# Performance work log

Measured on AMD Instinct MI355X. Metric: run time of the kernel, lower is better.

## Reference

```python
import jax, jax.numpy as jnp
import numpy as np

DIM = 1024
HEADS = 16
DIM_HEAD = 64
INNER = HEADS * DIM_HEAD
SCALE = DIM_HEAD ** -0.5


def rotate_half(t):
    # '... (j d) -> ... j d' with j=2: split last dim in half
    x1, x2 = jnp.split(t, 2, axis=-1)
    return jnp.concatenate((-x2, x1), axis=-1)


def rotary_pos(n, d, dtype):
    inv_freq = 1.0 / (10000.0 ** (jnp.arange(0, d, 2, dtype=jnp.float32) / d))
    freqs = jnp.arange(n, dtype=jnp.float32)[:, None] * inv_freq[None, :]  # (n, d/2)
    return jnp.concatenate((freqs, freqs), axis=-1).astype(dtype)  # (n, d)


def apply_rope(pos, t):
    return t * jnp.cos(pos) + rotate_half(t) * jnp.sin(pos)


def setup_inputs() -> dict:
    key = jax.random.key(0)
    ks = jax.random.split(key, 5)
    x = jax.random.normal(ks[0], (2, 2048, DIM), dtype=jnp.float32)
    gamma = jnp.ones((DIM,), dtype=jnp.float32)
    beta = jnp.zeros((DIM,), dtype=jnp.float32)
    Wq = jax.random.normal(ks[1], (DIM, INNER), dtype=jnp.float32) * 0.02
    Wkv = jax.random.normal(ks[2], (DIM, 2 * INNER), dtype=jnp.float32) * 0.02
    Wo = jax.random.normal(ks[3], (INNER, DIM), dtype=jnp.float32) * 0.02
    return {"x": x, "gamma": gamma, "beta": beta, "Wq": Wq, "Wkv": Wkv, "Wo": Wo}


def reference(x, gamma, beta, Wq, Wkv, Wo):
    b, n, _ = x.shape
    # LayerNorm with learned gamma, fixed-zero beta buffer
    mu = jnp.mean(x, axis=-1, keepdims=True)
    var = jnp.var(x, axis=-1, keepdims=True)
    xn = (x - mu) / jnp.sqrt(var + 1e-5) * gamma + beta

    q = xn @ Wq                       # (b, n, inner)
    kv = xn @ Wkv
    k, v = jnp.split(kv, 2, axis=-1)

    def to_heads(t):
        return t.reshape(b, n, HEADS, DIM_HEAD).transpose(0, 2, 1, 3)  # b h n d

    q, k, v = map(to_heads, (q, k, v))

    pos = rotary_pos(n, DIM_HEAD, x.dtype)  # (n, d)
    q = apply_rope(pos, q)
    k = apply_rope(pos, k)

    q = q * SCALE
    sim = jnp.einsum('bhid,bhjd->bhij', q, k)

    neg = -jnp.finfo(sim.dtype).max
    causal_mask = jnp.triu(jnp.ones((n, n), dtype=bool), k=1)
    sim = jnp.where(causal_mask, neg, sim)

    attn = jax.nn.softmax(sim, axis=-1)
    out = jnp.einsum('bhij,bhjd->bhid', attn, v)
    out = out.transpose(0, 2, 1, 3).reshape(b, n, INNER)
    return out @ Wo
```

## Files before the change

### kernel.cpp

```cpp
#include <hip/hip_runtime.h>
#include <stdint.h>

typedef unsigned short u16;
typedef __attribute__((ext_vector_type(8))) short short8;
typedef __attribute__((ext_vector_type(4))) float floatx4;
typedef __attribute__((ext_vector_type(4))) unsigned short u16x4;
typedef __attribute__((ext_vector_type(2))) unsigned int uint2v;

__device__ __forceinline__ float bf2f(u16 v) {
  union { uint32_t u; float f; } x; x.u = ((uint32_t)v) << 16; return x.f;
}
__device__ __forceinline__ u16 f2bf(float f) {
  union { float f; uint32_t u; } x; x.f = f;
  uint32_t r = x.u + 0x7fffu + ((x.u >> 16) & 1u);
  return (u16)(r >> 16);
}
__device__ __forceinline__ uint32_t fu(float f) {
  union { float f; uint32_t u; } x; x.f = f; return x.u;
}

#define GL2LDS(g, l)                                                          \
  __builtin_amdgcn_global_load_lds(                                           \
      (const __attribute__((address_space(1))) void*)(g),                     \
      (__attribute__((address_space(3))) void*)(l), 16, 0, 0)

__global__ __launch_bounds__(256) void prep_k(const float* __restrict__ x,
                                              const float* __restrict__ gamma,
                                              const float* __restrict__ beta,
                                              const float* __restrict__ Wq,
                                              const float* __restrict__ Wkv,
                                              const float* __restrict__ Wo,
                                              u16* __restrict__ xn,
                                              u16* __restrict__ wqkvT,
                                              u16* __restrict__ woT) {
  int bid = blockIdx.x;
  int t = threadIdx.x;
  if (bid < 4096) {
    int row = bid;
    const float* xr = x + (size_t)row * 1024;
    float4 xv = *(const float4*)(xr + t * 4);
    float v0 = xv.x, v1 = xv.y, v2 = xv.z, v3 = xv.w;
    float s = v0 + v1 + v2 + v3;
    float s2 = v0 * v0 + v1 * v1 + v2 * v2 + v3 * v3;
#pragma unroll
    for (int d = 1; d < 64; d <<= 1) {
      s += __shfl_xor(s, d, 64);
      s2 += __shfl_xor(s2, d, 64);
    }
    __shared__ float red[8];
    int lane = t & 63, wv = t >> 6;
    if (lane == 0) { red[wv] = s; red[4 + wv] = s2; }
    __syncthreads();
    s = red[0] + red[1] + red[2] + red[3];
    s2 = red[4] + red[5] + red[6] + red[7];
    float mu = s * (1.0f / 1024.0f);
    float var = s2 * (1.0f / 1024.0f) - mu * mu;
    float rstd = rsqrtf(var + 1e-5f);
    float4 gv = *(const float4*)(gamma + t * 4);
    float4 bv = *(const float4*)(beta + t * 4);
    u16x4 ov;
    ov.x = f2bf((v0 - mu) * rstd * gv.x + bv.x);
    ov.y = f2bf((v1 - mu) * rstd * gv.y + bv.y);
    ov.z = f2bf((v2 - mu) * rstd * gv.z + bv.z);
    ov.w = f2bf((v3 - mu) * rstd * gv.w + bv.w);
    *(u16x4*)(xn + (size_t)row * 1024 + t * 4) = ov;
  } else {
    __shared__ float tile[32][33];
    int wb = bid - 4096;
    const float* in;
    u16* outp;
    int C;
    if (wb < 1024) { in = Wq; outp = wqkvT; C = 1024; }
    else if (wb < 3072) { wb -= 1024; in = Wkv; outp = wqkvT + 1024 * 1024; C = 2048; }
    else { wb -= 3072; in = Wo; outp = woT; C = 1024; }
    int nbx = C >> 5;
    int c0 = (wb % nbx) * 32, r0 = (wb / nbx) * 32;
    int tx = t & 31, ty = t >> 5;
#pragma unroll
    for (int i = 0; i < 32; i += 8)
      tile[ty + i][tx] = in[(size_t)(r0 + ty + i) * C + c0 + tx];
    __syncthreads();
#pragma unroll
    for (int i = 0; i < 32; i += 8)
      outp[(size_t)(c0 + ty + i) * 1024 + r0 + tx] = f2bf(tile[tx][ty + i]);
  }
}

__global__ __launch_bounds__(256) void gemm_qkv_k(const u16* __restrict__ A,
                                                  const u16* __restrict__ BT,
                                                  u16* __restrict__ C) {
  const int K = 1024, lda = 1024, ldc = 3072;
  __shared__ __align__(16) u16 lA[2][128 * 32];
  __shared__ __align__(16) u16 lB[2][128 * 32];
  int tid = threadIdx.x;
  int bm = blockIdx.y * 128;
  int bn = blockIdx.x * 128;
  int w = tid >> 6, l = tid & 63;
  int wm = (w >> 1) * 64, wn = (w & 1) * 64;
  int lr = l & 15, lq = l >> 4;
  floatx4 acc[4][4] = {};
  int sr = w * 16 + (l >> 2);
  int sc = (l & 3) * 8;
  int sds = sr * 32 + sc;
  const u16* pA0 = A + (size_t)(bm + sr) * lda + sc;
  const u16* pA1 = pA0 + (size_t)64 * lda;
  const u16* pB0 = BT + (size_t)(bn + sr) * K + sc;
  const u16* pB1 = pB0 + (size_t)64 * K;
  int ao[4], bo[4];
#pragma unroll
  for (int i = 0; i < 4; i++) {
    ao[i] = (wm + i * 16 + lr) * 32 + lq * 8;
    bo[i] = (wn + i * 16 + lr) * 32 + lq * 8;
  }

#define STAGE_QKV(bi)                                                         \
  {                                                                           \
    GL2LDS(pA0, &lA[bi][sds]);                                                \
    GL2LDS(pA1, &lA[bi][sds + 2048]);                                         \
    GL2LDS(pB0, &lB[bi][sds]);                                                \
    GL2LDS(pB1, &lB[bi][sds + 2048]);                                         \
    pA0 += 32; pA1 += 32; pB0 += 32; pB1 += 32;                               \
  }
#define COMPUTE_QKV(bi)                                                       \
  {                                                                           \
    short8 afr[4], bfr[4];                                                    \
    _Pragma("unroll") for (int i = 0; i < 4; i++)                             \
        afr[i] = *(const short8*)(&lA[bi][ao[i]]);                            \
    _Pragma("unroll") for (int i = 0; i < 4; i++)                             \
        bfr[i] = *(const short8*)(&lB[bi][bo[i]]);                            \
    _Pragma("unroll") for (int mi = 0; mi < 4; mi++)                          \
        _Pragma("unroll") for (int ni = 0; ni < 4; ni++)                      \
            acc[mi][ni] = __builtin_amdgcn_mfma_f32_16x16x32_bf16(            \
                afr[mi], bfr[ni], acc[mi][ni], 0, 0, 0);                      \
  }

  STAGE_QKV(0);
  __syncthreads();
#pragma unroll 1
  for (int t = 0; t < 16; ++t) {
    STAGE_QKV(1);
    COMPUTE_QKV(0);
    __syncthreads();
    if (t < 15) STAGE_QKV(0);
    COMPUTE_QKV(1);
    __syncthreads();
  }

  int sec = bn >> 10;
  if (sec == 2) {
#pragma unroll
    for (int mi = 0; mi < 4; mi++)
#pragma unroll
      for (int ni = 0; ni < 4; ni++) {
        int col = bn + wn + ni * 16 + lr;
        int cv = col - 2048;
        int row = bm + wm + mi * 16 + lq * 4;
        int bq = row >> 11;
        int n = row & 2047;
        int bh = (bq << 4) | (cv >> 6);
        int d = cv & 63;
        size_t L = ((size_t)(bh * 64 + d) << 11) + n;
        u16x4 ov;
        ov.x = f2bf(acc[mi][ni][0]);
        ov.y = f2bf(acc[mi][ni][1]);
        ov.z = f2bf(acc[mi][ni][2]);
        ov.w = f2bf(acc[mi][ni][3]);
        *(u16x4*)(C + (L >> 10) * 3072 + 2048 + (L & 1023)) = ov;
      }
  } else {
    float QS = (sec == 0) ? 0.125f * 1.44269504088896f : 1.0f;
#pragma unroll
    for (int ni = 0; ni < 2; ni++) {
      int i = ni * 16 + lr;
      float invf = exp2f(-(float)i * 0.4152410118609203f);
#pragma unroll
      for (int mi = 0; mi < 4; mi++)
#pragma unroll
        for (int r = 0; r < 4; r++) {
          int row = bm + wm + mi * 16 + lq * 4 + r;
          int n = row & 2047;
          float ang = (float)n * invf;
          float s_, c_;
          __sincosf(ang, &s_, &c_);
          float x1 = acc[mi][ni][r], x2 = acc[mi][ni + 2][r];
          int col = bn + wn + ni * 16 + lr;
          C[(size_t)row * ldc + col] = f2bf((x1 * c_ - x2 * s_) * QS);
          C[(size_t)row * ldc + col + 32] = f2bf((x2 * c_ + x1 * s_) * QS);
        }
    }
  }
}

__global__ __launch_bounds__(256) void gemm64_bf16_k(const u16* __restrict__ A,
                                                     const u16* __restrict__ BT,
                                                     float* __restrict__ C,
                                                     int K, int lda, int ldc) {
  __shared__ __align__(16) u16 lA[2][64 * 32];
  __shared__ __align__(16) u16 lB[2][128 * 32];
  int tid = threadIdx.x;
  int bm = blockIdx.y * 64;
  int bn = blockIdx.x * 128;
  int w = tid >> 6, l = tid & 63;
  int wm = (w >> 1) * 32, wn = (w & 1) * 64;
  int lr = l & 15, lq = l >> 4;
  floatx4 acc[2][4] = {};
  int sr = w * 16 + (l >> 2);
  int sc = (l & 3) * 8;
  int sds = sr * 32 + sc;
  const u16* pA0 = A + (size_t)(bm + sr) * lda + sc;
  const u16* pB0 = BT + (size_t)(bn + sr) * K + sc;
  const u16* pB1 = pB0 + (size_t)64 * K;
  int ao[2], bo[4];
#pragma unroll
  for (int i = 0; i < 2; i++) ao[i] = (wm + i * 16 + lr) * 32 + lq * 8;
#pragma unroll
  for (int i = 0; i < 4; i++) bo[i] = (wn + i * 16 + lr) * 32 + lq * 8;

#define STAGE_O(bi)                                                           \
  {                                                                           \
    GL2LDS(pA0, &lA[bi][sds]);                                                \
    GL2LDS(pB0, &lB[bi][sds]);                                                \
    GL2LDS(pB1, &lB[bi][sds + 2048]);                                         \
    pA0 += 32; pB0 += 32; pB1 += 32;                                          \
  }
#define COMPUTE_O(bi)                                                         \
  {                                                                           \
    short8 afr[2], bfr[4];                                                    \
    _Pragma("unroll") for (int i = 0; i < 2; i++)                             \
        afr[i] = *(const short8*)(&lA[bi][ao[i]]);                            \
    _Pragma("unroll") for (int i = 0; i < 4; i++)                             \
        bfr[i] = *(const short8*)(&lB[bi][bo[i]]);                            \
    _Pragma("unroll") for (int mi = 0; mi < 2; mi++)                          \
        _Pragma("unroll") for (int ni = 0; ni < 4; ni++)                      \
            acc[mi][ni] = __builtin_amdgcn_mfma_f32_16x16x32_bf16(            \
                afr[mi], bfr[ni], acc[mi][ni], 0, 0, 0);                      \
  }

  int NT2 = K >> 6;
  STAGE_O(0);
  __syncthreads();
#pragma unroll 1
  for (int t = 0; t < NT2; ++t) {
    STAGE_O(1);
    COMPUTE_O(0);
    __syncthreads();
    if (t < NT2 - 1) STAGE_O(0);
    COMPUTE_O(1);
    __syncthreads();
  }
#pragma unroll
  for (int mi = 0; mi < 2; mi++)
#pragma unroll
    for (int ni = 0; ni < 4; ni++)
#pragma unroll
      for (int r = 0; r < 4; r++) {
        int row = bm + wm + mi * 16 + lq * 4 + r;
        int col = bn + wn + ni * 16 + lr;
        C[(size_t)row * ldc + col] = acc[mi][ni][r];
      }
}

#define LPT 64
#define FIXM 4.0f
__device__ __forceinline__ void attn_tile2(const u16* lK, const u16* lV, u16* lp,
                                           const short8* aq, floatx4* o,
                                           float& l_i, int lr, int lq,
                                           bool diag, int q0, int k0g,
                                           short8 ones) {
  floatx4 s[4];
  __builtin_amdgcn_s_setprio(1);
#pragma unroll
  for (int ni = 0; ni < 4; ni++) {
    floatx4 a = {};
#pragma unroll
    for (int kc = 0; kc < 2; kc++) {
      int R = ni * 16 + lr;
      int c8 = (kc * 4 + lq) ^ (R & 7);
      short8 kf = *(const short8*)&lK[R * 64 + c8 * 8];
      a = __builtin_amdgcn_mfma_f32_16x16x32_bf16(kf, aq[kc], a, 0, 0, 0);
    }
    s[ni] = a;
  }
  __builtin_amdgcn_s_setprio(0);
  if (diag) {
    int qg = q0 + lr;
#pragma unroll
    for (int ni = 0; ni < 4; ni++)
#pragma unroll
      for (int r = 0; r < 4; r++) {
        int kg = k0g + ni * 16 + lq * 4 + r;
        if (kg > qg) s[ni][r] = -1e30f;
      }
  }
  int swz = (lr & 7) << 3;
#pragma unroll
  for (int ni = 0; ni < 4; ni++) {
    float p0 = exp2f(s[ni][0] - FIXM), p1 = exp2f(s[ni][1] - FIXM);
    float p2 = exp2f(s[ni][2] - FIXM), p3 = exp2f(s[ni][3] - FIXM);
    uint2v dw;
    dw.x = __builtin_amdgcn_perm(fu(p1), fu(p0), 0x07060302u);
    dw.y = __builtin_amdgcn_perm(fu(p3), fu(p2), 0x07060302u);
    *(uint2v*)&lp[lr * LPT + ((ni * 16 + lq * 4) ^ swz)] = dw;
  }
  short8 pb0 = *(const short8*)&lp[lr * LPT + ((lq * 8) ^ swz)];
  short8 pb1 = *(const short8*)&lp[lr * LPT + ((32 + lq * 8) ^ swz)];
  __builtin_amdgcn_s_setprio(1);
  floatx4 z = {};
  z = __builtin_amdgcn_mfma_f32_16x16x32_bf16(ones, pb0, z, 0, 0, 0);
  z = __builtin_amdgcn_mfma_f32_16x16x32_bf16(ones, pb1, z, 0, 0, 0);
  l_i += z[0];
#pragma unroll
  for (int di = 0; di < 4; di++) {
    int R = di * 16 + lr;
    int c80 = lq ^ (R & 7);
    int c81 = (4 + lq) ^ (R & 7);
    short8 v0 = *(const short8*)&lV[R * 64 + c80 * 8];
    o[di] = __builtin_amdgcn_mfma_f32_16x16x32_bf16(v0, pb0, o[di], 0, 0, 0);
    short8 v1 = *(const short8*)&lV[R * 64 + c81 * 8];
    o[di] = __builtin_amdgcn_mfma_f32_16x16x32_bf16(v1, pb1, o[di], 0, 0, 0);
  }
  __builtin_amdgcn_s_setprio(0);
}

__global__ __launch_bounds__(256) void attn_k(const u16* __restrict__ qkv,
                                              u16* __restrict__ out) {
  __shared__ __align__(16) u16 lK[2][64 * 64];
  __shared__ __align__(16) u16 lV[2][64 * 64];
  __shared__ __align__(16) u16 lP[4][16 * LPT];
  int bh = blockIdx.x;
  int b = bh >> 4, h = bh & 15;
  int y = blockIdx.y;
  int g = y >> 3, o_ = y & 7;
  int j = (g & 1) ? ((g << 3) + 7 - o_) : y;
  int tid = threadIdx.x;
  int w = tid >> 6, l = tid & 63;
  int lr = l & 15, lq = l >> 4;
  int q0 = j * 64 + w * 16;
  const u16* qb = qkv + (size_t)b * 2048 * 3072 + h * 64;
  const u16* kb = qkv + (size_t)b * 2048 * 3072 + 1024 + h * 64;
  int bh64 = bh * 64;
  short8 aq[2];
  aq[0] = *(const short8*)(qb + (size_t)(q0 + lr) * 3072 + lq * 8);
  aq[1] = *(const short8*)(qb + (size_t)(q0 + lr) * 3072 + 32 + lq * 8);
  short8 ones;
#pragma unroll
  for (int i = 0; i < 8; i++) ones[i] = (short)0x3F80;
  floatx4 o[4] = {};
  float l_ = 0.0f;
  int srow8 = l >> 3;
  int sc8 = (l & 7) ^ srow8;
  u16* lp = &lP[w][0];
  auto stage = [&](int bufi, int kt) {
#pragma unroll
    for (int c = 0; c < 2; c++) {
      int m = w + c * 4;
      int row = m * 8 + srow8;
      GL2LDS(kb + (size_t)(kt * 64 + row) * 3072 + sc8 * 8, &lK[bufi][m * 512]);
      int nn = kt * 64 + sc8 * 8;
      GL2LDS(qkv + (size_t)((bh64 + row) * 2 + (nn >> 10)) * 3072 + 2048 +
                 (nn & 1023),
             &lV[bufi][m * 512]);
    }
  };
  stage(0, 0);
  for (int kt = 0; kt <= j; ++kt) {
    int cur = kt & 1;
    __syncthreads();
    if (kt < j) stage(cur ^ 1, kt + 1);
    attn_tile2(lK[cur], lV[cur], lp, aq, o, l_, lr, lq, kt == j, q0, kt * 64,
               ones);
  }
  float rl = 1.0f / l_;
#pragma unroll
  for (int di = 0; di < 4; di++) {
    uint2v dw;
    u16 a0 = f2bf(o[di][0] * rl), a1 = f2bf(o[di][1] * rl);
    u16 a2 = f2bf(o[di][2] * rl), a3 = f2bf(o[di][3] * rl);
    dw.x = (uint32_t)a0 | ((uint32_t)a1 << 16);
    dw.y = (uint32_t)a2 | ((uint32_t)a3 << 16);
    int dcol = h * 64 + di * 16 + lq * 4;
    *(uint2v*)(out + ((size_t)(b * 2048 + q0 + lr)) * 1024 + dcol) = dw;
  }
}

extern "C" void kernel_launch(void* const* d_in, const int* in_sizes, int n_in,
                              void* d_out, int out_size, void* d_ws, size_t ws_size,
                              hipStream_t stream) {
  const float* x = (const float*)d_in[0];
  const float* gamma = (const float*)d_in[1];
  const float* beta = (const float*)d_in[2];
  const float* Wq = (const float*)d_in[3];
  const float* Wkv = (const float*)d_in[4];
  const float* Wo = (const float*)d_in[5];
  float* out = (float*)d_out;
  char* ws = (char*)d_ws;

  u16* qkv = (u16*)(ws);
  u16* wqkvT = (u16*)(ws + 25165824);
  u16* woT = (u16*)(ws + 31457280);
  u16* xn = (u16*)(ws + 33554432);
  u16* attn_out = xn;

  prep_k<<<8192, 256, 0, stream>>>(x, gamma, beta, Wq, Wkv, Wo, xn, wqkvT, woT);
  gemm_qkv_k<<<dim3(24, 32), 256, 0, stream>>>(xn, wqkvT, qkv);
  attn_k<<<dim3(32, 32), 256, 0, stream>>>(qkv, attn_out);
  gemm64_bf16_k<<<dim3(8, 64), 256, 0, stream>>>(attn_out, woT, out, 1024, 1024, 1024);
}
```

Before: 204.1 us.

## Triple-buffer GEMM LDS staging with vmcnt-based barriers and drop attention setprio

Both GEMM kernels move from double to triple-buffered LDS staging. Each iteration now prefetches two tiles ahead and waits only on the older loads with a partial s_waitcnt vmcnt plus barrier, replacing the full __syncthreads. This is meant to hide global-to-LDS latency better, at the cost of more LDS per block and hardcoded trip counts (the O-projection loop now assumes K=1024). The attention tile also drops its s_setprio hints around the MFMA sections.

Result: faster. 196.1 us (-3.9%).

```diff
diff --git a/kernel.cpp b/kernel.cpp
--- a/kernel.cpp
+++ b/kernel.cpp
@@ -23,6 +23,9 @@
   __builtin_amdgcn_global_load_lds(                                           \
       (const __attribute__((address_space(1))) void*)(g),                     \
       (__attribute__((address_space(3))) void*)(l), 16, 0, 0)
+
+#define WAITBAR(N)                                                            \
+  asm volatile("s_waitcnt vmcnt(" #N ")\n\ts_barrier" ::: "memory")
 
 __global__ __launch_bounds__(256) void prep_k(const float* __restrict__ x,
                                               const float* __restrict__ gamma,
@@ -90,8 +93,8 @@
                                                   const u16* __restrict__ BT,
                                                   u16* __restrict__ C) {
   const int K = 1024, lda = 1024, ldc = 3072;
-  __shared__ __align__(16) u16 lA[2][128 * 32];
-  __shared__ __align__(16) u16 lB[2][128 * 32];
+  __shared__ __align__(16) u16 lA[3][128 * 32];
+  __shared__ __align__(16) u16 lB[3][128 * 32];
   int tid = threadIdx.x;
   int bm = blockIdx.y * 128;
   int bn = blockIdx.x * 128;
@@ -135,16 +138,15 @@
   }
 
   STAGE_QKV(0);
-  __syncthreads();
+  STAGE_QKV(1);
 #pragma unroll 1
-  for (int t = 0; t < 16; ++t) {
-    STAGE_QKV(1);
-    COMPUTE_QKV(0);
-    __syncthreads();
-    if (t < 15) STAGE_QKV(0);
-    COMPUTE_QKV(1);
-    __syncthreads();
-  }
+  for (int t = 0; t < 10; ++t) {
+    WAITBAR(4); STAGE_QKV(2); COMPUTE_QKV(0);
+    WAITBAR(4); STAGE_QKV(0); COMPUTE_QKV(1);
+    WAITBAR(4); STAGE_QKV(1); COMPUTE_QKV(2);
+  }
+  WAITBAR(4); COMPUTE_QKV(0);
+  WAITBAR(0); COMPUTE_QKV(1);
 
   int sec = bn >> 10;
   if (sec == 2) {
@@ -195,8 +197,8 @@
                                                      const u16* __restrict__ BT,
                                                      float* __restrict__ C,
                                                      int K, int lda, int ldc) {
-  __shared__ __align__(16) u16 lA[2][64 * 32];
-  __shared__ __align__(16) u16 lB[2][128 * 32];
+  __shared__ __align__(16) u16 lA[3][64 * 32];
+  __shared__ __align__(16) u16 lB[3][128 * 32];
   int tid = threadIdx.x;
   int bm = blockIdx.y * 64;
   int bn = blockIdx.x * 128;
@@ -236,18 +238,17 @@
                 afr[mi], bfr[ni], acc[mi][ni], 0, 0, 0);                      \
   }
 
-  int NT2 = K >> 6;
   STAGE_O(0);
-  __syncthreads();
+  STAGE_O(1);
 #pragma unroll 1
-  for (int t = 0; t < NT2; ++t) {
-    STAGE_O(1);
-    COMPUTE_O(0);
-    __syncthreads();
-    if (t < NT2 - 1) STAGE_O(0);
-    COMPUTE_O(1);
-    __syncthreads();
-  }
+  for (int t = 0; t < 10; ++t) {
+    WAITBAR(3); STAGE_O(2); COMPUTE_O(0);
+    WAITBAR(3); STAGE_O(0); COMPUTE_O(1);
+    WAITBAR(3); STAGE_O(1); COMPUTE_O(2);
+  }
+  WAITBAR(3); COMPUTE_O(0);
+  WAITBAR(0); COMPUTE_O(1);
+
 #pragma unroll
   for (int mi = 0; mi < 2; mi++)
 #pragma unroll
@@ -268,7 +269,6 @@
                                            bool diag, int q0, int k0g,
                                            short8 ones) {
   floatx4 s[4];
-  __builtin_amdgcn_s_setprio(1);
 #pragma unroll
   for (int ni = 0; ni < 4; ni++) {
     floatx4 a = {};
@@ -281,7 +281,6 @@
     }
     s[ni] = a;
   }
-  __builtin_amdgcn_s_setprio(0);
   if (diag) {
     int qg = q0 + lr;
 #pragma unroll
@@ -304,7 +303,6 @@
   }
   short8 pb0 = *(const short8*)&lp[lr * LPT + ((lq * 8) ^ swz)];
   short8 pb1 = *(const short8*)&lp[lr * LPT + ((32 + lq * 8) ^ swz)];
-  __builtin_amdgcn_s_setprio(1);
   floatx4 z = {};
   z = __builtin_amdgcn_mfma_f32_16x16x32_bf16(ones, pb0, z, 0, 0, 0);
   z = __builtin_amdgcn_mfma_f32_16x16x32_bf16(ones, pb1, z, 0, 0, 0);
@@ -319,7 +317,6 @@
     short8 v1 = *(const short8*)&lV[R * 64 + c81 * 8];
     o[di] = __builtin_amdgcn_mfma_f32_16x16x32_bf16(v1, pb1, o[di], 0, 0, 0);
   }
-  __builtin_amdgcn_s_setprio(0);
 }
 
 __global__ __launch_bounds__(256) void attn_k(const u16* __restrict__ qkv,
```
